# Performance work log

Hardware: AMD Instinct MI355X
Metric: run time of the kernel (lower is better)

The kernel has to match this reference:

```python
import jax, jax.numpy as jnp
import numpy as np

N, D, K = 262144, 64, 512


def setup_inputs() -> dict:
    key = jax.random.key(0)
    k1, k2 = jax.random.split(key)
    x = jax.random.normal(k1, (N, D), dtype=jnp.float32)
    # embedding initialized uniform(-1/K, 1/K) as in the torch module
    codebook = jax.random.uniform(k2, (K, D), dtype=jnp.float32, minval=-1.0 / K, maxval=1.0 / K)
    return {"x": x, "codebook": codebook}


def reference(x, codebook):
    # distances[n,k] = ||x_n||^2 + ||w_k||^2 - 2 x_n . w_k  (cdist^2 via matmul)
    d = (jnp.sum(x * x, axis=1, keepdims=True)
         + jnp.sum(codebook * codebook, axis=1)
         - 2.0 * jnp.matmul(x, codebook.T))  # [N, K]
    indices = jnp.argmin(d, axis=1)          # [N]
    x_q = codebook[indices]                  # [N, D] gather
    commitment_loss = jnp.mean((jax.lax.stop_gradient(x_q) - x) ** 2)
    embedding_loss = jnp.mean((x_q - jax.lax.stop_gradient(x)) ** 2)
    vq_loss = commitment_loss * 0.25 + embedding_loss
    # straight-through estimator
    x_out = x + jax.lax.stop_gradient(x_q - x)
    return (x_out, vq_loss)
```

## Files before the change

kernel.cpp:

```cpp
#include <hip/hip_runtime.h>

#define N_ROWS 262144
#define DIM    64
#define KCB    512

#define ABLOCKS  1024
#define ATHREADS 512
#define BTHREADS 256
#define BBLOCKS  ((N_ROWS * 16) / BTHREADS)

typedef float f32x4 __attribute__((ext_vector_type(4)));

__device__ inline float dot4(float4 a) {
    return a.x * a.x + a.y * a.y + a.z * a.z + a.w * a.w;
}
__device__ inline unsigned umin2(unsigned a, unsigned b) { return a < b ? a : b; }

__device__ inline long pk8(float4 f0, float4 f1, float s) {
    int lo = 0, hi = 0;
    lo = __builtin_amdgcn_cvt_pk_fp8_f32(f0.x * s, f0.y * s, lo, false);
    lo = __builtin_amdgcn_cvt_pk_fp8_f32(f0.z * s, f0.w * s, lo, true);
    hi = __builtin_amdgcn_cvt_pk_fp8_f32(f1.x * s, f1.y * s, hi, false);
    hi = __builtin_amdgcn_cvt_pk_fp8_f32(f1.z * s, f1.w * s, hi, true);
    return (long)(((unsigned long)(unsigned)hi << 32) | (unsigned)lo);
}

__global__ __launch_bounds__(ATHREADS, 2) void vq_score(
    const float* __restrict__ x, const float* __restrict__ cb,
    unsigned short* __restrict__ idx, float* __restrict__ partials)
{
    __shared__ long   cb8_sh[KCB * 8];
    __shared__ f32x4  wn_sh4[KCB / 4];
    __shared__ float  red_sh[8];

    const int tid    = threadIdx.x;
    const int lane   = tid & 63;
    const int wave   = tid >> 6;
    const int lane15 = lane & 15;
    const int half   = lane >> 4;

    const int wrow = blockIdx.x * 256 + wave * 32;
    const float* xc = x + (size_t)(wrow + lane15) * DIM + half * 8;

    float4 p00 = *(const float4*)xc,        p01 = *(const float4*)(xc + 4);
    float4 p02 = *(const float4*)(xc + 32), p03 = *(const float4*)(xc + 36);

    #pragma unroll
    for (int it = 0; it < (KCB * 8) / ATHREADS; ++it) {
        const int fg = tid + it * ATHREADS;
        const int row = fg >> 3, g = fg & 7;
        const float* src = cb + row * DIM + g * 8;
        float4 f0 = *(const float4*)src;
        float4 f1 = *(const float4*)(src + 4);
        float sq = dot4(f0) + dot4(f1);
        sq += __shfl_xor(sq, 1);
        sq += __shfl_xor(sq, 2);
        sq += __shfl_xor(sq, 4);
        const int slot = ((row >> 1) << 4) + ((row & 1) << 3)
                       + (g ^ ((row >> 1) & 7));
        cb8_sh[slot] = pk8(f0, f1, -256.0f);
        if (g == 0) ((float*)wn_sh4)[row] = 256.0f + 128.0f * sq;
    }

    float xn0 = dot4(p00) + dot4(p01) + dot4(p02) + dot4(p03);
    long b0lo = pk8(p00, p01, 1.0f), b0hi = pk8(p02, p03, 1.0f);
    __syncthreads();

    float4 q00 = *(const float4*)(xc + 1024), q01 = *(const float4*)(xc + 1028);
    float4 q02 = *(const float4*)(xc + 1056), q03 = *(const float4*)(xc + 1060);

    const int key  = (lane15 >> 1) & 7;
    const int base = (lane15 >> 1) * 16 + (lane15 & 1) * 8;
    const int slo  = base + (half ^ key);
    const int shi  = slo ^ 4;
    const unsigned hb   = (unsigned)(half * 4);
    const unsigned mask = 0xFFFFFE00u;

    float lossAcc = 0.f;
    long blo = b0lo, bhi = b0hi;
    float xn = xn0;

    #pragma unroll
    for (int ch = 0; ch < 2; ++ch) {
        if (ch == 1) {
            xn  = dot4(q00) + dot4(q01) + dot4(q02) + dot4(q03);
            blo = pk8(q00, q01, 1.0f);
            bhi = pk8(q02, q03, 1.0f);
        }
        unsigned u0 = 0xFFFFFFFFu;

        #pragma unroll 8
        for (int t = 0; t < 32; ++t) {
            long  alo = cb8_sh[t * 128 + slo];
            long  ahi = cb8_sh[t * 128 + shi];
            f32x4 wnv = wn_sh4[t * 4 + half];
            const unsigned kb = (unsigned)(t * 16) | hb;

            f32x4 acc = wnv;
            acc = __builtin_amdgcn_mfma_f32_16x16x32_fp8_fp8(alo, blo, acc, 0, 0, 0);
            acc = __builtin_amdgcn_mfma_f32_16x16x32_fp8_fp8(ahi, bhi, acc, 0, 0, 0);
            unsigned p0 = (__float_as_uint(acc[0]) & mask) | kb;
            unsigned p1 = (__float_as_uint(acc[1]) & mask) | (kb | 1u);
            unsigned p2 = (__float_as_uint(acc[2]) & mask) | (kb | 2u);
            unsigned p3 = (__float_as_uint(acc[3]) & mask) | (kb | 3u);
            u0 = umin2(u0, umin2(umin2(p0, p1), umin2(p2, p3)));
        }

        unsigned f0 = u0;
        f0 = umin2(f0, (unsigned)__shfl_xor((int)f0, 16));
        f0 = umin2(f0, (unsigned)__shfl_xor((int)f0, 32));
        float xs = xn;
        xs += __shfl_xor(xs, 16); xs += __shfl_xor(xs, 32);

        float pf = __uint_as_float(f0 & mask);
        lossAcc += 0.25f * (xs + pf * (1.0f / 128.0f) - 2.0f);

        if (lane < 16) idx[wrow + ch * 16 + lane] = (unsigned short)(f0 & 511u);
    }

    #pragma unroll
    for (int off = 1; off < 64; off <<= 1) lossAcc += __shfl_xor(lossAcc, off);
    if (lane == 0) red_sh[wave] = lossAcc;
    __syncthreads();
    if (tid == 0) {
        float s = 0.f;
        #pragma unroll
        for (int w = 0; w < 8; ++w) s += red_sh[w];
        partials[blockIdx.x] = s;
    }
}

__global__ __launch_bounds__(BTHREADS, 8) void vq_gather(
    const unsigned short* __restrict__ idx, const float* __restrict__ cb,
    float* __restrict__ out)
{
    const int g   = blockIdx.x * BTHREADS + threadIdx.x;
    const int row = g >> 4;
    const int dq  = g & 15;
    const int k   = (int)idx[row];
    const f32x4* cb4 = (const f32x4*)cb;
    ((f32x4*)out)[g] = cb4[k * 16 + dq];
}

__global__ void vq_finalize(const float* __restrict__ partials,
                            float* __restrict__ out_loss) {
    __shared__ float sh[256];
    int t = threadIdx.x;
    sh[t] = partials[t] + partials[t + 256] + partials[t + 512] + partials[t + 768];
    __syncthreads();
    #pragma unroll
    for (int s = 128; s > 0; s >>= 1) {
        if (t < s) sh[t] += sh[t + s];
        __syncthreads();
    }
    if (t == 0) out_loss[0] = sh[0] * (1.25f / (float)(N_ROWS * DIM));
}

extern "C" void kernel_launch(void* const* d_in, const int* in_sizes, int n_in,
                              void* d_out, int out_size, void* d_ws, size_t ws_size,
                              hipStream_t stream) {
    const float* x  = (const float*)d_in[0];
    const float* cb = (const float*)d_in[1];
    float* out      = (float*)d_out;
    float* partials = (float*)d_ws;
    unsigned short* idx = (unsigned short*)((char*)d_ws + 4096);

    hipLaunchKernelGGL(vq_score, dim3(ABLOCKS), dim3(ATHREADS), 0, stream,
                       x, cb, idx, partials);
    hipLaunchKernelGGL(vq_gather, dim3(BBLOCKS), dim3(BTHREADS), 0, stream,
                       idx, cb, out);
    hipLaunchKernelGGL(vq_finalize, dim3(1), dim3(256), 0, stream,
                       partials, out + (size_t)N_ROWS * DIM);
}
```

Before: 48.16 us.

## Fuse codebook gather into scoring kernel and precompute FP8 codebook image once

Moves the fp8 packing of the codebook and its squared norms into a small prep kernel that writes a swizzled image to workspace, so each scoring block only copies that image into LDS. The gather of the chosen codebook rows is fused into the scoring kernel, which drops the separate gather launch and the index round trip through global memory. Blocks shrink to 4 waves, each handling 64 rows in four chunks with the next chunk's x loads prefetched. The argmin switches from unsigned integer min to float min on the packed keys. This adds a kernel launch for prep and puts more serial work per wave.

```diff
diff --git a/kernel.cpp b/kernel.cpp
--- a/kernel.cpp
+++ b/kernel.cpp
@@ -4,10 +4,8 @@
 #define DIM    64
 #define KCB    512
 
-#define ABLOCKS  1024
-#define ATHREADS 512
-#define BTHREADS 256
-#define BBLOCKS  ((N_ROWS * 16) / BTHREADS)
+#define MBLOCKS  1024
+#define MTHREADS 256
 
 typedef float f32x4 __attribute__((ext_vector_type(4)));
 
@@ -25,13 +23,30 @@
     return (long)(((unsigned long)(unsigned)hi << 32) | (unsigned)lo);
 }
 
-__global__ __launch_bounds__(ATHREADS, 2) void vq_score(
+__global__ void vq_prep(const float* __restrict__ cb, long* __restrict__ cb8,
+                        float* __restrict__ wn) {
+    const int fg  = blockIdx.x * 512 + threadIdx.x;
+    const int row = fg >> 3, g = fg & 7;
+    const float* src = cb + row * DIM + g * 8;
+    float4 f0 = *(const float4*)src;
+    float4 f1 = *(const float4*)(src + 4);
+    float sq = dot4(f0) + dot4(f1);
+    sq += __shfl_xor(sq, 1);
+    sq += __shfl_xor(sq, 2);
+    sq += __shfl_xor(sq, 4);
+    const int slot = ((row >> 1) << 4) + ((row & 1) << 3)
+                   + (g ^ ((row >> 1) & 7));
+    cb8[slot] = pk8(f0, f1, -256.0f);
+    if (g == 0) wn[row] = 256.0f + 128.0f * sq;
+}
+
+__global__ __launch_bounds__(MTHREADS, 4) void vq_main(
     const float* __restrict__ x, const float* __restrict__ cb,
-    unsigned short* __restrict__ idx, float* __restrict__ partials)
+    const f32x4* __restrict__ img_g, float* __restrict__ out,
+    float* __restrict__ partials)
 {
-    __shared__ long   cb8_sh[KCB * 8];
-    __shared__ f32x4  wn_sh4[KCB / 4];
-    __shared__ float  red_sh[8];
+    __shared__ f32x4 img[2176];
+    __shared__ float red_sh[4];
 
     const int tid    = threadIdx.x;
     const int lane   = tid & 63;
@@ -39,35 +54,23 @@
     const int lane15 = lane & 15;
     const int half   = lane >> 4;
 
-    const int wrow = blockIdx.x * 256 + wave * 32;
+    const int wrow = blockIdx.x * 256 + wave * 64;
     const float* xc = x + (size_t)(wrow + lane15) * DIM + half * 8;
 
-    float4 p00 = *(const float4*)xc,        p01 = *(const float4*)(xc + 4);
-    float4 p02 = *(const float4*)(xc + 32), p03 = *(const float4*)(xc + 36);
+    float4 a0 = *(const float4*)xc,        a1 = *(const float4*)(xc + 4);
+    float4 a2 = *(const float4*)(xc + 32), a3 = *(const float4*)(xc + 36);
 
     #pragma unroll
-    for (int it = 0; it < (KCB * 8) / ATHREADS; ++it) {
-        const int fg = tid + it * ATHREADS;
-        const int row = fg >> 3, g = fg & 7;
-        const float* src = cb + row * DIM + g * 8;
-        float4 f0 = *(const float4*)src;
-        float4 f1 = *(const float4*)(src + 4);
-        float sq = dot4(f0) + dot4(f1);
-        sq += __shfl_xor(sq, 1);
-        sq += __shfl_xor(sq, 2);
-        sq += __shfl_xor(sq, 4);
-        const int slot = ((row >> 1) << 4) + ((row & 1) << 3)
-                       + (g ^ ((row >> 1) & 7));
-        cb8_sh[slot] = pk8(f0, f1, -256.0f);
-        if (g == 0) ((float*)wn_sh4)[row] = 256.0f + 128.0f * sq;
-    }
+    for (int it = 0; it < 8; ++it)
+        img[tid + it * 256] = img_g[tid + it * 256];
+    if (tid < 128) img[2048 + tid] = img_g[2048 + tid];
 
-    float xn0 = dot4(p00) + dot4(p01) + dot4(p02) + dot4(p03);
-    long b0lo = pk8(p00, p01, 1.0f), b0hi = pk8(p02, p03, 1.0f);
+    float xn = dot4(a0) + dot4(a1) + dot4(a2) + dot4(a3);
+    long blo = pk8(a0, a1, 1.0f), bhi = pk8(a2, a3, 1.0f);
     __syncthreads();
 
-    float4 q00 = *(const float4*)(xc + 1024), q01 = *(const float4*)(xc + 1028);
-    float4 q02 = *(const float4*)(xc + 1056), q03 = *(const float4*)(xc + 1060);
+    const long*  cb8 = (const long*)img;
+    const f32x4* wn4 = img + 2048;
 
     const int key  = (lane15 >> 1) & 7;
     const int base = (lane15 >> 1) * 16 + (lane15 & 1) * 8;
@@ -77,45 +80,58 @@
     const unsigned mask = 0xFFFFFE00u;
 
     float lossAcc = 0.f;
-    long blo = b0lo, bhi = b0hi;
-    float xn = xn0;
+    float4 n0, n1, n2, n3;
 
     #pragma unroll
-    for (int ch = 0; ch < 2; ++ch) {
-        if (ch == 1) {
-            xn  = dot4(q00) + dot4(q01) + dot4(q02) + dot4(q03);
-            blo = pk8(q00, q01, 1.0f);
-            bhi = pk8(q02, q03, 1.0f);
+    for (int ch = 0; ch < 4; ++ch) {
+        if (ch < 3) {
+            const float* xp = xc + (ch + 1) * 1024;
+            n0 = *(const float4*)xp;        n1 = *(const float4*)(xp + 4);
+            n2 = *(const float4*)(xp + 32); n3 = *(const float4*)(xp + 36);
         }
-        unsigned u0 = 0xFFFFFFFFu;
 
+        float run = __uint_as_float(0x7F7FFFFFu);
         #pragma unroll 8
         for (int t = 0; t < 32; ++t) {
-            long  alo = cb8_sh[t * 128 + slo];
-            long  ahi = cb8_sh[t * 128 + shi];
-            f32x4 wnv = wn_sh4[t * 4 + half];
+            long  alo = cb8[t * 128 + slo];
+            long  ahi = cb8[t * 128 + shi];
+            f32x4 wnv = wn4[t * 4 + half];
             const unsigned kb = (unsigned)(t * 16) | hb;
 
             f32x4 acc = wnv;
             acc = __builtin_amdgcn_mfma_f32_16x16x32_fp8_fp8(alo, blo, acc, 0, 0, 0);
             acc = __builtin_amdgcn_mfma_f32_16x16x32_fp8_fp8(ahi, bhi, acc, 0, 0, 0);
-            unsigned p0 = (__float_as_uint(acc[0]) & mask) | kb;
-            unsigned p1 = (__float_as_uint(acc[1]) & mask) | (kb | 1u);
-            unsigned p2 = (__float_as_uint(acc[2]) & mask) | (kb | 2u);
-            unsigned p3 = (__float_as_uint(acc[3]) & mask) | (kb | 3u);
-            u0 = umin2(u0, umin2(umin2(p0, p1), umin2(p2, p3)));
+            float p0 = __uint_as_float((__float_as_uint(acc[0]) & mask) | kb);
+            float p1 = __uint_as_float((__float_as_uint(acc[1]) & mask) | (kb | 1u));
+            float p2 = __uint_as_float((__float_as_uint(acc[2]) & mask) | (kb | 2u));
+            float p3 = __uint_as_float((__float_as_uint(acc[3]) & mask) | (kb | 3u));
+            run = fminf(fminf(fminf(p0, p1), p2), fminf(run, p3));
         }
 
-        unsigned f0 = u0;
-        f0 = umin2(f0, (unsigned)__shfl_xor((int)f0, 16));
-        f0 = umin2(f0, (unsigned)__shfl_xor((int)f0, 32));
+        run = fminf(run, __shfl_xor(run, 16));
+        run = fminf(run, __shfl_xor(run, 32));
         float xs = xn;
         xs += __shfl_xor(xs, 16); xs += __shfl_xor(xs, 32);
 
+        const unsigned f0 = __float_as_uint(run);
         float pf = __uint_as_float(f0 & mask);
         lossAcc += 0.25f * (xs + pf * (1.0f / 128.0f) - 2.0f);
+        const int bk0 = (int)(f0 & 511u);
 
-        if (lane < 16) idx[wrow + ch * 16 + lane] = (unsigned short)(f0 & 511u);
+        float* outw = out + (size_t)(wrow + ch * 16) * DIM;
+        #pragma unroll
+        for (int j = 0; j < 4; ++j) {
+            const int srcl = (j * 4 + half) & 15;
+            int bk = __shfl(bk0, srcl);
+            f32x4 qv = *(const f32x4*)(cb + (size_t)bk * DIM + lane15 * 4);
+            *(f32x4*)(outw + j * 256 + lane * 4) = qv;
+        }
+
+        if (ch < 3) {
+            xn  = dot4(n0) + dot4(n1) + dot4(n2) + dot4(n3);
+            blo = pk8(n0, n1, 1.0f);
+            bhi = pk8(n2, n3, 1.0f);
+        }
     }
 
     #pragma unroll
@@ -123,23 +139,9 @@
     if (lane == 0) red_sh[wave] = lossAcc;
     __syncthreads();
     if (tid == 0) {
-        float s = 0.f;
-        #pragma unroll
-        for (int w = 0; w < 8; ++w) s += red_sh[w];
+        float s = red_sh[0] + red_sh[1] + red_sh[2] + red_sh[3];
         partials[blockIdx.x] = s;
     }
-}
-
-__global__ __launch_bounds__(BTHREADS, 8) void vq_gather(
-    const unsigned short* __restrict__ idx, const float* __restrict__ cb,
-    float* __restrict__ out)
-{
-    const int g   = blockIdx.x * BTHREADS + threadIdx.x;
-    const int row = g >> 4;
-    const int dq  = g & 15;
-    const int k   = (int)idx[row];
-    const f32x4* cb4 = (const f32x4*)cb;
-    ((f32x4*)out)[g] = cb4[k * 16 + dq];
 }
 
 __global__ void vq_finalize(const float* __restrict__ partials,
@@ -162,13 +164,13 @@
     const float* x  = (const float*)d_in[0];
     const float* cb = (const float*)d_in[1];
     float* out      = (float*)d_out;
-    float* partials = (float*)d_ws;
-    unsigned short* idx = (unsigned short*)((char*)d_ws + 4096);
+    long*  ws_cb8   = (long*)d_ws;
+    float* ws_wn    = (float*)((char*)d_ws + 32768);
+    float* partials = (float*)((char*)d_ws + 36864);
 
-    hipLaunchKernelGGL(vq_score, dim3(ABLOCKS), dim3(ATHREADS), 0, stream,
-                       x, cb, idx, partials);
-    hipLaunchKernelGGL(vq_gather, dim3(BBLOCKS), dim3(BTHREADS), 0, stream,
-                       idx, cb, out);
+    hipLaunchKernelGGL(vq_prep, dim3(8), dim3(512), 0, stream, cb, ws_cb8, ws_wn);
+    hipLaunchKernelGGL(vq_main, dim3(MBLOCKS), dim3(MTHREADS), 0, stream,
+                       x, cb, (const f32x4*)d_ws, out, partials);
     hipLaunchKernelGGL(vq_finalize, dim3(1), dim3(256), 0, stream,
                        partials, out + (size_t)N_ROWS * DIM);
 }
```

Measured after the change: 40.33 us. -16.3%, faster.
